# Kernel optimization log

Hardware: AMD Instinct MI355X
Metric: run time of the kernel (lower is better)

## Reference

```python
import jax, jax.numpy as jnp
import numpy as np

B, T, C, HS = 8, 4096, 1024, 64  # batch, seq, n_embd, head_size


def setup_inputs() -> dict:
    key = jax.random.key(0)
    kx, kk, kq, kv = jax.random.split(key, 4)
    x = jax.random.normal(kx, (B, T, C), dtype=jnp.float32)
    # bias-free linear weights, stored as [in, out] like flax kernels
    s = 1.0 / np.sqrt(C)
    Wk = jax.random.normal(kk, (C, HS), dtype=jnp.float32) * s
    Wq = jax.random.normal(kq, (C, HS), dtype=jnp.float32) * s
    Wv = jax.random.normal(kv, (C, HS), dtype=jnp.float32) * s
    return {"x": x, "Wk": Wk, "Wq": Wq, "Wv": Wv}


def reference(x, Wk, Wq, Wv):
    # x: [B, T, C]
    Tq = x.shape[1]
    Cdim = x.shape[2]
    k = jnp.einsum('btc,ch->bth', x, Wk)  # [B,T,HS]
    q = jnp.einsum('btc,ch->bth', x, Wq)
    v = jnp.einsum('btc,ch->bth', x, Wv)
    # NOTE: original scales by C**-0.5 (full embed dim), not head_size**-0.5
    scale = Cdim ** (-0.5)
    wei = jnp.einsum('bth,bsh->bts', q, k) * scale  # [B,T,T]
    causal = jnp.tril(jnp.ones((Tq, Tq), dtype=bool))
    wei = jnp.where(causal, wei, -jnp.inf)
    wei = jax.nn.softmax(wei, axis=-1)
    out = jnp.einsum('bts,bsh->bth', wei, v)  # [B,T,HS]
    return out
```

## Files before the change

kernel.cpp:

```cpp
#include <hip/hip_runtime.h>
#include <hip/hip_bf16.h>


typedef __attribute__((ext_vector_type(8))) short short8;
typedef __attribute__((ext_vector_type(4))) float f32x4;

#define NB 8
#define NT 4096
#define NC 1024
#define NH 64

__device__ __forceinline__ unsigned short f2bf(float f) {
    unsigned int u = __builtin_bit_cast(unsigned int, f);
    u += 0x7fffu + ((u >> 16) & 1u);
    return (unsigned short)(u >> 16);
}

__device__ __forceinline__ unsigned cvt_pk_bf16(float lo, float hi) {
    unsigned r;
    asm("v_cvt_pk_bf16_f32 %0, %1, %2" : "=v"(r) : "v"(lo), "v"(hi));
    return r;
}

#define GLOAD16(gp, lp)                                                        \
    __builtin_amdgcn_global_load_lds(                                          \
        (const __attribute__((address_space(1))) void*)(gp),                   \
        (__attribute__((address_space(3))) void*)(lp), 16, 0, 0)

__global__ __launch_bounds__(256) void wprep_kernel(
    const float* __restrict__ Wk, const float* __restrict__ Wq,
    const float* __restrict__ Wv, unsigned short* __restrict__ Wt)
{
    int n = blockIdx.x;
    int which = n >> 6, h = n & 63;
    const float* W = (which == 0) ? Wk : (which == 1) ? Wq : Wv;
    for (int c = threadIdx.x; c < NC; c += 256)
        Wt[(size_t)n * NC + c] = f2bf(W[(size_t)c * NH + h]);
}

__global__ __launch_bounds__(256, 2) void proj_kernel(
    const float* __restrict__ x, const unsigned short* __restrict__ Wt,
    unsigned short* __restrict__ qws, unsigned short* __restrict__ kws,
    unsigned short* __restrict__ vtws)
{
    __shared__ char lds[4][20480];

    const int lane = threadIdx.x & 63;
    const int wave = threadIdx.x >> 6;
    const int l15 = lane & 15;
    const int kg = lane >> 4;
    const int m0 = blockIdx.x * 64;

    const int agS = (lane & 7) ^ (lane >> 3);
    const float* aSrc[2];
#pragma unroll
    for (int j = 0; j < 2; ++j) {
        int i = wave * 2 + j;
        int r = 8 * i + (lane >> 3);
        aSrc[j] = x + (size_t)(m0 + r) * NC + agS * 4;
    }
    const int bgS = (lane & 3) ^ ((lane >> 2) & 3);
    const unsigned short* bSrc[3];
#pragma unroll
    for (int j = 0; j < 3; ++j) {
        int u = wave * 3 + j;
        int r = 16 * u + (lane >> 2);
        bSrc[j] = Wt + (size_t)r * NC + bgS * 8;
    }

    f32x4 acc[12];
#pragma unroll
    for (int i = 0; i < 12; ++i) acc[i] = f32x4{0.f, 0.f, 0.f, 0.f};

#define STAGE_CHUNK(c)                                                         \
    do {                                                                       \
        char* base_ = lds[(c) & 3];                                            \
        _Pragma("unroll")                                                      \
        for (int j = 0; j < 2; ++j)                                            \
            GLOAD16(aSrc[j] + (c) * 32, base_ + (wave * 2 + j) * 1024);        \
        _Pragma("unroll")                                                      \
        for (int j = 0; j < 3; ++j)                                            \
            GLOAD16(bSrc[j] + (c) * 32, base_ + 8192 + (wave * 3 + j) * 1024); \
    } while (0)

    STAGE_CHUNK(0);
    STAGE_CHUNK(1);

    for (int kc = 0; kc < 32; ++kc) {
        if (kc < 30) {
            STAGE_CHUNK(kc + 2);
            asm volatile("s_waitcnt vmcnt(10)" ::: "memory");
        } else if (kc == 30) {
            asm volatile("s_waitcnt vmcnt(5)" ::: "memory");
        } else {
            asm volatile("s_waitcnt vmcnt(0)" ::: "memory");
        }
        __builtin_amdgcn_sched_barrier(0);
        __builtin_amdgcn_s_barrier();

        const char* Ab = lds[kc & 3];
        const char* Bb = lds[kc & 3] + 8192;
        {
            const int r = wave * 16 + l15;
            const int g0 = kg * 2;
            f32x4 a0 = *(const f32x4*)(Ab + r * 128 + ((g0 ^ (r & 7)) * 16));
            f32x4 a1 = *(const f32x4*)(Ab + r * 128 + (((g0 + 1) ^ (r & 7)) * 16));
            short8 a;
            a[0] = (short)f2bf(a0[0]); a[1] = (short)f2bf(a0[1]);
            a[2] = (short)f2bf(a0[2]); a[3] = (short)f2bf(a0[3]);
            a[4] = (short)f2bf(a1[0]); a[5] = (short)f2bf(a1[1]);
            a[6] = (short)f2bf(a1[2]); a[7] = (short)f2bf(a1[3]);
#pragma unroll
            for (int nt = 0; nt < 12; ++nt) {
                int rb = nt * 16 + l15;
                short8 bfrag = *(const short8*)(
                    Bb + rb * 64 + ((kg ^ (rb & 3)) * 16));
                acc[nt] = __builtin_amdgcn_mfma_f32_16x16x32_bf16(a, bfrag, acc[nt], 0, 0, 0);
            }
        }
    }
#undef STAGE_CHUNK

    const float cs = 0.04508422f;
    const int crow0 = m0 + wave * 16 + (kg << 2);
#pragma unroll
    for (int nt = 0; nt < 12; ++nt) {
        int n = nt * 16 + l15;
        int which = n >> 6;
        int h = n & 63;
#pragma unroll
        for (int r = 0; r < 4; ++r) {
            int gm = crow0 + r;
            float av = acc[nt][r];
            if (which == 1) av *= cs;
            unsigned short v = f2bf(av);
            if (which == 0) {
                kws[(size_t)gm * NH + h] = v;
            } else if (which == 1) {
                qws[(size_t)gm * NH + h] = v;
            } else {
                int bb = gm >> 12, tt = gm & 4095;
                vtws[((size_t)(bb * NH + h)) * NT + tt] = v;
            }
        }
    }
}

__global__ __launch_bounds__(256) void flash_kernel(
    const unsigned short* __restrict__ qws, const unsigned short* __restrict__ kws,
    const unsigned short* __restrict__ vtws,
    float* __restrict__ opart, float* __restrict__ mlpart)
{
    __shared__ unsigned short Kbuf[2][64 * 64];
    __shared__ unsigned short Vbuf[2][64 * 64];
    __shared__ unsigned short Plds[4 * 16 * 64];

    const int id = blockIdx.x;
    const int kvh = id >> 9;
    const int rem9 = id & 511;
    const int lighthalf = rem9 >> 8;
    const int rem = rem9 & 255;
    const int b = rem & 7;
    const int i32 = rem >> 3;
    const int qt = lighthalf ? i32 : (63 - i32);
    const int nkv = qt + 1;
    const int hsp = nkv - (nkv >> 1);
    const int k0 = kvh ? hsp : 0;
    const int k1 = kvh ? nkv : hsp;
    const int pid_ = (kvh << 9) | ((b << 6) | qt);

    float* mlp = mlpart + (size_t)pid_ * 128;
    float* op  = opart + (size_t)pid_ * 4096;

    if (k0 >= k1) {
        f32x4 z = f32x4{0.f, 0.f, 0.f, 0.f};
        f32x4* op4 = (f32x4*)op;
        for (int i = threadIdx.x; i < 1024; i += 256) op4[i] = z;
        if (threadIdx.x < 64) {
            mlp[threadIdx.x] = -INFINITY;
            mlp[64 + threadIdx.x] = 0.f;
        }
        return;
    }

    const int lane = threadIdx.x & 63;
    const int wave = threadIdx.x >> 6;
    const int l15 = lane & 15;
    const int kg = lane >> 4;

    const int sg = (lane & 7) ^ (lane >> 3);
    const unsigned short* kSrc[2];
    const unsigned short* vSrc[2];
#pragma unroll
    for (int j = 0; j < 2; ++j) {
        int r = 16 * wave + 8 * j + (lane >> 3);
        kSrc[j] = kws + ((size_t)(b * NT) + r) * NH + sg * 8;
        vSrc[j] = vtws + ((size_t)(b * NH + r)) * NT + sg * 8;
    }

    short8 qf[2];
    {
        const unsigned short* qp =
            qws + ((size_t)(b * NT + qt * 64 + wave * 16 + l15)) * NH + kg * 8;
        qf[0] = *(const short8*)(qp);
        qf[1] = *(const short8*)(qp + 32);
    }

    f32x4 o[4];
#pragma unroll
    for (int dt = 0; dt < 4; ++dt) o[dt] = f32x4{0.f, 0.f, 0.f, 0.f};
    float m_r = -INFINITY;
    float l_r = 0.f;

    char* pw = (char*)Plds + wave * 2048;
    const int pswz = (l15 & 7) << 4;

#pragma unroll
    for (int j = 0; j < 2; ++j) {
        int i = 2 * wave + j;
        GLOAD16(kSrc[j] + (size_t)k0 * 64 * NH, (char*)Kbuf[0] + i * 1024);
        GLOAD16(vSrc[j] + (size_t)k0 * 64,      (char*)Vbuf[0] + i * 1024);
    }
    __syncthreads();

    int cur = 0;
    for (int kv = k0; kv < k1; ++kv) {
        if (kv + 1 < k1) {
#pragma unroll
            for (int j = 0; j < 2; ++j) {
                int i = 2 * wave + j;
                GLOAD16(kSrc[j] + (size_t)(kv + 1) * 64 * NH,
                        (char*)Kbuf[cur ^ 1] + i * 1024);
                GLOAD16(vSrc[j] + (size_t)(kv + 1) * 64,
                        (char*)Vbuf[cur ^ 1] + i * 1024);
            }
        }

        const char* Kb = (const char*)Kbuf[cur];
        const char* Vb = (const char*)Vbuf[cur];

        f32x4 st[4];
#pragma unroll
        for (int jt = 0; jt < 4; ++jt) st[jt] = f32x4{0.f, 0.f, 0.f, 0.f};
#pragma unroll
        for (int ks = 0; ks < 2; ++ks) {
            const int cbb = ks * 64 + kg * 16;
#pragma unroll
            for (int jt = 0; jt < 4; ++jt) {
                int krow = jt * 16 + l15;
                short8 kf = *(const short8*)(Kb + krow * 128 +
                                             (cbb ^ ((krow & 7) << 4)));
                st[jt] = __builtin_amdgcn_mfma_f32_16x16x32_bf16(kf, qf[ks], st[jt], 0, 0, 0);
            }
        }

        if (kv == qt) {
#pragma unroll
            for (int jt = 0; jt < 4; ++jt)
#pragma unroll
                for (int r = 0; r < 4; ++r)
                    if (jt * 16 + (kg << 2) + r > wave * 16 + l15)
                        st[jt][r] = -1e30f;
        }

        float lmax;
        {
            float t0 = fmaxf(fmaxf(st[0][0], st[0][1]), fmaxf(st[0][2], st[0][3]));
            float t1 = fmaxf(fmaxf(st[1][0], st[1][1]), fmaxf(st[1][2], st[1][3]));
            float t2 = fmaxf(fmaxf(st[2][0], st[2][1]), fmaxf(st[2][2], st[2][3]));
            float t3 = fmaxf(fmaxf(st[3][0], st[3][1]), fmaxf(st[3][2], st[3][3]));
            lmax = fmaxf(fmaxf(t0, t1), fmaxf(t2, t3));
        }

        if (!__all(lmax <= m_r + 8.0f)) {
            float pmax = lmax;
            pmax = fmaxf(pmax, __shfl_xor(pmax, 16));
            pmax = fmaxf(pmax, __shfl_xor(pmax, 32));
            float mn = fmaxf(m_r, pmax);
            float alpha = __builtin_amdgcn_exp2f(m_r - mn);
            m_r = mn;
            l_r *= alpha;
#pragma unroll
            for (int dt = 0; dt < 4; ++dt)
#pragma unroll
                for (int r = 0; r < 4; ++r)
                    o[dt][r] *= alpha;
        }

#pragma unroll
        for (int jt = 0; jt < 4; ++jt)
#pragma unroll
            for (int r = 0; r < 4; ++r)
                st[jt][r] = __builtin_amdgcn_exp2f(st[jt][r] - m_r);
        {
            float t0 = (st[0][0] + st[0][1]) + (st[0][2] + st[0][3]);
            float t1 = (st[1][0] + st[1][1]) + (st[1][2] + st[1][3]);
            float t2 = (st[2][0] + st[2][1]) + (st[2][2] + st[2][3]);
            float t3 = (st[3][0] + st[3][1]) + (st[3][2] + st[3][3]);
            l_r += (t0 + t1) + (t2 + t3);
        }

#pragma unroll
        for (int jt = 0; jt < 4; ++jt) {
            unsigned w0 = cvt_pk_bf16(st[jt][0], st[jt][1]);
            unsigned w1 = cvt_pk_bf16(st[jt][2], st[jt][3]);
            uint2 t; t.x = w0; t.y = w1;
            *(uint2*)(pw + l15 * 128 + ((jt * 32 + kg * 8) ^ pswz)) = t;
        }
        short8 pf[2];
#pragma unroll
        for (int ks = 0; ks < 2; ++ks)
            pf[ks] = *(const short8*)(pw + l15 * 128 + ((ks * 64 + kg * 16) ^ pswz));

#pragma unroll
        for (int ks = 0; ks < 2; ++ks) {
            const int cbb = ks * 64 + kg * 16;
#pragma unroll
            for (int dt = 0; dt < 4; ++dt) {
                int vrow = dt * 16 + l15;
                short8 vf = *(const short8*)(Vb + vrow * 128 +
                                             (cbb ^ ((vrow & 7) << 4)));
                o[dt] = __builtin_amdgcn_mfma_f32_16x16x32_bf16(vf, pf[ks], o[dt], 0, 0, 0);
            }
        }

        __syncthreads();
        cur ^= 1;
    }

    float lsum = l_r;
    lsum += __shfl_xor(lsum, 16);
    lsum += __shfl_xor(lsum, 32);
    float* orow = op + (wave * 16 + l15) * 64 + (kg << 2);
#pragma unroll
    for (int dt = 0; dt < 4; ++dt)
        *(f32x4*)(orow + dt * 16) = o[dt];
    if (kg == 0) {
        int q = wave * 16 + l15;
        mlp[q] = m_r;
        mlp[64 + q] = lsum;
    }
}

__global__ __launch_bounds__(256) void combine_kernel(
    const float* __restrict__ opart, const float* __restrict__ mlpart,
    float* __restrict__ out)
{
    const int cid = blockIdx.x;
    const int b = cid >> 6, qt = cid & 63;
    const float* mlA = mlpart + (size_t)cid * 128;
    const float* mlB = mlpart + (size_t)(512 + cid) * 128;
    const f32x4* oA = (const f32x4*)(opart + (size_t)cid * 4096);
    const f32x4* oB = (const f32x4*)(opart + (size_t)(512 + cid) * 4096);
    f32x4* og = (f32x4*)out;

#pragma unroll
    for (int i = 0; i < 4; ++i) {
        int g = threadIdx.x + i * 256;
        int row = g >> 4;
        float mA = mlA[row], lA = mlA[64 + row];
        float mB = mlB[row], lB = mlB[64 + row];
        float ms = fmaxf(mA, mB);
        float eA = __builtin_amdgcn_exp2f(mA - ms);
        float eB = __builtin_amdgcn_exp2f(mB - ms);
        float dinv = __builtin_amdgcn_rcpf(eA * lA + eB * lB);
        f32x4 a = oA[g], c = oB[g];
        f32x4 r;
        r[0] = (eA * a[0] + eB * c[0]) * dinv;
        r[1] = (eA * a[1] + eB * c[1]) * dinv;
        r[2] = (eA * a[2] + eB * c[2]) * dinv;
        r[3] = (eA * a[3] + eB * c[3]) * dinv;
        og[((size_t)(b * NT) + qt * 64 + row) * 16 + (g & 15)] = r;
    }
}

extern "C" void kernel_launch(void* const* d_in, const int* in_sizes, int n_in,
                              void* d_out, int out_size, void* d_ws, size_t ws_size,
                              hipStream_t stream) {
    const float* x  = (const float*)d_in[0];
    const float* Wk = (const float*)d_in[1];
    const float* Wq = (const float*)d_in[2];
    const float* Wv = (const float*)d_in[3];
    float* out = (float*)d_out;

    unsigned short* ws   = (unsigned short*)d_ws;
    const size_t qkv_elems = (size_t)NB * NT * NH;
    unsigned short* qws  = ws;
    unsigned short* kws  = qws + qkv_elems;
    unsigned short* vtws = kws + qkv_elems;
    unsigned short* Wt   = vtws + qkv_elems;
    float* opart  = (float*)(Wt + (size_t)192 * NC);
    float* mlpart = opart + (size_t)1024 * 4096;

    wprep_kernel<<<dim3(192), dim3(256), 0, stream>>>(Wk, Wq, Wv, Wt);
    proj_kernel<<<dim3(512), dim3(256), 0, stream>>>(x, Wt, qws, kws, vtws);
    flash_kernel<<<dim3(1024), dim3(256), 0, stream>>>(qws, kws, vtws, opart, mlpart);
    combine_kernel<<<dim3(512), dim3(256), 0, stream>>>(opart, mlpart, out);
}
```

Baseline: 86.96 us.

## Fuse split-KV combine into flash kernel via atomic last-arriver merge

New measurement: 242.1 us. 2.78x slower.

```diff
diff --git a/kernel.cpp b/kernel.cpp
--- a/kernel.cpp
+++ b/kernel.cpp
@@ -29,9 +29,11 @@
 
 __global__ __launch_bounds__(256) void wprep_kernel(
     const float* __restrict__ Wk, const float* __restrict__ Wq,
-    const float* __restrict__ Wv, unsigned short* __restrict__ Wt)
+    const float* __restrict__ Wv, unsigned short* __restrict__ Wt,
+    int* __restrict__ flags)
 {
     int n = blockIdx.x;
+    if (n < 2) flags[n * 256 + threadIdx.x] = 0;
     int which = n >> 6, h = n & 63;
     const float* W = (which == 0) ? Wk : (which == 1) ? Wq : Wv;
     for (int c = threadIdx.x; c < NC; c += 256)
@@ -149,11 +151,13 @@
 __global__ __launch_bounds__(256) void flash_kernel(
     const unsigned short* __restrict__ qws, const unsigned short* __restrict__ kws,
     const unsigned short* __restrict__ vtws,
-    float* __restrict__ opart, float* __restrict__ mlpart)
+    float* __restrict__ opart, float* __restrict__ mlpart,
+    int* __restrict__ flags, float* __restrict__ out)
 {
     __shared__ unsigned short Kbuf[2][64 * 64];
     __shared__ unsigned short Vbuf[2][64 * 64];
     __shared__ unsigned short Plds[4 * 16 * 64];
+    __shared__ int role;
 
     const int id = blockIdx.x;
     const int kvh = id >> 9;
@@ -172,17 +176,6 @@
     float* mlp = mlpart + (size_t)pid_ * 128;
     float* op  = opart + (size_t)pid_ * 4096;
 
-    if (k0 >= k1) {
-        f32x4 z = f32x4{0.f, 0.f, 0.f, 0.f};
-        f32x4* op4 = (f32x4*)op;
-        for (int i = threadIdx.x; i < 1024; i += 256) op4[i] = z;
-        if (threadIdx.x < 64) {
-            mlp[threadIdx.x] = -INFINITY;
-            mlp[64 + threadIdx.x] = 0.f;
-        }
-        return;
-    }
-
     const int lane = threadIdx.x & 63;
     const int wave = threadIdx.x >> 6;
     const int l15 = lane & 15;
@@ -215,11 +208,12 @@
     char* pw = (char*)Plds + wave * 2048;
     const int pswz = (l15 & 7) << 4;
 
+    const int kst = (k0 < 64) ? k0 : 63;
 #pragma unroll
     for (int j = 0; j < 2; ++j) {
         int i = 2 * wave + j;
-        GLOAD16(kSrc[j] + (size_t)k0 * 64 * NH, (char*)Kbuf[0] + i * 1024);
-        GLOAD16(vSrc[j] + (size_t)k0 * 64,      (char*)Vbuf[0] + i * 1024);
+        GLOAD16(kSrc[j] + (size_t)kst * 64 * NH, (char*)Kbuf[0] + i * 1024);
+        GLOAD16(vSrc[j] + (size_t)kst * 64,      (char*)Vbuf[0] + i * 1024);
     }
     __syncthreads();
 
@@ -242,6 +236,7 @@
         f32x4 st[4];
 #pragma unroll
         for (int jt = 0; jt < 4; ++jt) st[jt] = f32x4{0.f, 0.f, 0.f, 0.f};
+        __builtin_amdgcn_s_setprio(1);
 #pragma unroll
         for (int ks = 0; ks < 2; ++ks) {
             const int cbb = ks * 64 + kg * 16;
@@ -253,6 +248,7 @@
                 st[jt] = __builtin_amdgcn_mfma_f32_16x16x32_bf16(kf, qf[ks], st[jt], 0, 0, 0);
             }
         }
+        __builtin_amdgcn_s_setprio(0);
 
         if (kv == qt) {
 #pragma unroll
@@ -312,6 +308,7 @@
         for (int ks = 0; ks < 2; ++ks)
             pf[ks] = *(const short8*)(pw + l15 * 128 + ((ks * 64 + kg * 16) ^ pswz));
 
+        __builtin_amdgcn_s_setprio(1);
 #pragma unroll
         for (int ks = 0; ks < 2; ++ks) {
             const int cbb = ks * 64 + kg * 16;
@@ -323,6 +320,7 @@
                 o[dt] = __builtin_amdgcn_mfma_f32_16x16x32_bf16(vf, pf[ks], o[dt], 0, 0, 0);
             }
         }
+        __builtin_amdgcn_s_setprio(0);
 
         __syncthreads();
         cur ^= 1;
@@ -331,46 +329,43 @@
     float lsum = l_r;
     lsum += __shfl_xor(lsum, 16);
     lsum += __shfl_xor(lsum, 32);
-    float* orow = op + (wave * 16 + l15) * 64 + (kg << 2);
+    const int q = wave * 16 + l15;
+    float* orow = op + q * 64 + (kg << 2);
 #pragma unroll
     for (int dt = 0; dt < 4; ++dt)
         *(f32x4*)(orow + dt * 16) = o[dt];
     if (kg == 0) {
-        int q = wave * 16 + l15;
         mlp[q] = m_r;
         mlp[64 + q] = lsum;
     }
-}
-
-__global__ __launch_bounds__(256) void combine_kernel(
-    const float* __restrict__ opart, const float* __restrict__ mlpart,
-    float* __restrict__ out)
-{
-    const int cid = blockIdx.x;
-    const int b = cid >> 6, qt = cid & 63;
-    const float* mlA = mlpart + (size_t)cid * 128;
-    const float* mlB = mlpart + (size_t)(512 + cid) * 128;
-    const f32x4* oA = (const f32x4*)(opart + (size_t)cid * 4096);
-    const f32x4* oB = (const f32x4*)(opart + (size_t)(512 + cid) * 4096);
-    f32x4* og = (f32x4*)out;
-
-#pragma unroll
-    for (int i = 0; i < 4; ++i) {
-        int g = threadIdx.x + i * 256;
-        int row = g >> 4;
-        float mA = mlA[row], lA = mlA[64 + row];
-        float mB = mlB[row], lB = mlB[64 + row];
-        float ms = fmaxf(mA, mB);
-        float eA = __builtin_amdgcn_exp2f(mA - ms);
-        float eB = __builtin_amdgcn_exp2f(mB - ms);
-        float dinv = __builtin_amdgcn_rcpf(eA * lA + eB * lB);
-        f32x4 a = oA[g], c = oB[g];
-        f32x4 r;
-        r[0] = (eA * a[0] + eB * c[0]) * dinv;
-        r[1] = (eA * a[1] + eB * c[1]) * dinv;
-        r[2] = (eA * a[2] + eB * c[2]) * dinv;
-        r[3] = (eA * a[3] + eB * c[3]) * dinv;
-        og[((size_t)(b * NT) + qt * 64 + row) * 16 + (g & 15)] = r;
+
+    __threadfence();
+    __syncthreads();
+    if (threadIdx.x == 0)
+        role = atomicAdd(&flags[(b << 6) | qt], 1);
+    __syncthreads();
+    if (role == 0) return;
+
+    __threadfence();
+    const int partner = pid_ ^ (1 << 9);
+    const float* mlP = mlpart + (size_t)partner * 128;
+    const float* opP = opart + (size_t)partner * 4096;
+    float mP = mlP[q], lP = mlP[64 + q];
+    float ms = fmaxf(m_r, mP);
+    float eO = __builtin_amdgcn_exp2f(m_r - ms);
+    float eP = __builtin_amdgcn_exp2f(mP - ms);
+    float dinv = __builtin_amdgcn_rcpf(eO * lsum + eP * lP);
+    const float* prow = opP + q * 64 + (kg << 2);
+    float* grow = out + ((size_t)(b * NT) + qt * 64 + q) * NH + (kg << 2);
+#pragma unroll
+    for (int dt = 0; dt < 4; ++dt) {
+        f32x4 pv = *(const f32x4*)(prow + dt * 16);
+        f32x4 rr;
+        rr[0] = (eO * o[dt][0] + eP * pv[0]) * dinv;
+        rr[1] = (eO * o[dt][1] + eP * pv[1]) * dinv;
+        rr[2] = (eO * o[dt][2] + eP * pv[2]) * dinv;
+        rr[3] = (eO * o[dt][3] + eP * pv[3]) * dinv;
+        *(f32x4*)(grow + dt * 16) = rr;
     }
 }
 
@@ -391,9 +386,9 @@
     unsigned short* Wt   = vtws + qkv_elems;
     float* opart  = (float*)(Wt + (size_t)192 * NC);
     float* mlpart = opart + (size_t)1024 * 4096;
-
-    wprep_kernel<<<dim3(192), dim3(256), 0, stream>>>(Wk, Wq, Wv, Wt);
+    int*   flags  = (int*)(mlpart + (size_t)1024 * 128);
+
+    wprep_kernel<<<dim3(192), dim3(256), 0, stream>>>(Wk, Wq, Wv, Wt, flags);
     proj_kernel<<<dim3(512), dim3(256), 0, stream>>>(x, Wt, qws, kws, vtws);
-    flash_kernel<<<dim3(1024), dim3(256), 0, stream>>>(qws, kws, vtws, opart, mlpart);
-    combine_kernel<<<dim3(512), dim3(256), 0, stream>>>(opart, mlpart, out);
-}
+    flash_kernel<<<dim3(1024), dim3(256), 0, stream>>>(qws, kws, vtws, opart, mlpart, flags, out);
+}
```

## Use 32-wide KV tiles with 4-stage ring buffer and finer split-K balance

Applied to the files above, without the earlier changes.

Result: slower. 96.44 us (+10.9%).

```diff
diff --git a/kernel.cpp b/kernel.cpp
--- a/kernel.cpp
+++ b/kernel.cpp
@@ -151,9 +151,9 @@
     const unsigned short* __restrict__ vtws,
     float* __restrict__ opart, float* __restrict__ mlpart)
 {
-    __shared__ unsigned short Kbuf[2][64 * 64];
-    __shared__ unsigned short Vbuf[2][64 * 64];
-    __shared__ unsigned short Plds[4 * 16 * 64];
+    __shared__ unsigned short Kbuf[4][32 * 64];
+    __shared__ unsigned short Vbuf[4][64 * 32];
+    __shared__ unsigned short Plds[4][16 * 32];
 
     const int id = blockIdx.x;
     const int kvh = id >> 9;
@@ -163,40 +163,24 @@
     const int b = rem & 7;
     const int i32 = rem >> 3;
     const int qt = lighthalf ? i32 : (63 - i32);
-    const int nkv = qt + 1;
-    const int hsp = nkv - (nkv >> 1);
-    const int k0 = kvh ? hsp : 0;
-    const int k1 = kvh ? nkv : hsp;
+    const int k0 = kvh ? (qt + 1) : 0;
+    const int k1 = kvh ? (2 * qt + 2) : (qt + 1);
     const int pid_ = (kvh << 9) | ((b << 6) | qt);
 
     float* mlp = mlpart + (size_t)pid_ * 128;
     float* op  = opart + (size_t)pid_ * 4096;
-
-    if (k0 >= k1) {
-        f32x4 z = f32x4{0.f, 0.f, 0.f, 0.f};
-        f32x4* op4 = (f32x4*)op;
-        for (int i = threadIdx.x; i < 1024; i += 256) op4[i] = z;
-        if (threadIdx.x < 64) {
-            mlp[threadIdx.x] = -INFINITY;
-            mlp[64 + threadIdx.x] = 0.f;
-        }
-        return;
-    }
 
     const int lane = threadIdx.x & 63;
     const int wave = threadIdx.x >> 6;
     const int l15 = lane & 15;
     const int kg = lane >> 4;
 
-    const int sg = (lane & 7) ^ (lane >> 3);
-    const unsigned short* kSrc[2];
-    const unsigned short* vSrc[2];
-#pragma unroll
-    for (int j = 0; j < 2; ++j) {
-        int r = 16 * wave + 8 * j + (lane >> 3);
-        kSrc[j] = kws + ((size_t)(b * NT) + r) * NH + sg * 8;
-        vSrc[j] = vtws + ((size_t)(b * NH + r)) * NT + sg * 8;
-    }
+    const unsigned short* kSrc =
+        kws + ((size_t)(b * NT) + 8 * wave + (lane >> 3)) * NH +
+        (((lane & 7) ^ (lane >> 3)) * 8);
+    const unsigned short* vSrc =
+        vtws + ((size_t)(b * NH) + 16 * wave + (lane >> 2)) * NT +
+        (((lane & 3) ^ ((lane >> 2) & 3)) * 8);
 
     short8 qf[2];
     {
@@ -205,6 +189,7 @@
         qf[0] = *(const short8*)(qp);
         qf[1] = *(const short8*)(qp + 32);
     }
+    asm volatile("s_waitcnt vmcnt(0)" ::: "memory");
 
     f32x4 o[4];
 #pragma unroll
@@ -212,54 +197,56 @@
     float m_r = -INFINITY;
     float l_r = 0.f;
 
-    char* pw = (char*)Plds + wave * 2048;
-    const int pswz = (l15 & 7) << 4;
-
-#pragma unroll
-    for (int j = 0; j < 2; ++j) {
-        int i = 2 * wave + j;
-        GLOAD16(kSrc[j] + (size_t)k0 * 64 * NH, (char*)Kbuf[0] + i * 1024);
-        GLOAD16(vSrc[j] + (size_t)k0 * 64,      (char*)Vbuf[0] + i * 1024);
-    }
-    __syncthreads();
-
-    int cur = 0;
+    char* pw = (char*)Plds[wave];
+    const int qbw = qt * 64 + wave * 16;
+
+#define STAGE_KV(t)                                                            \
+    do {                                                                       \
+        GLOAD16(kSrc + (size_t)(t) * 32 * NH, (char*)Kbuf[(t) & 3] + wave * 1024); \
+        GLOAD16(vSrc + (t) * 32,              (char*)Vbuf[(t) & 3] + wave * 1024); \
+    } while (0)
+
+    STAGE_KV(k0);
+    if (k0 + 1 < k1) STAGE_KV(k0 + 1);
+
     for (int kv = k0; kv < k1; ++kv) {
-        if (kv + 1 < k1) {
-#pragma unroll
-            for (int j = 0; j < 2; ++j) {
-                int i = 2 * wave + j;
-                GLOAD16(kSrc[j] + (size_t)(kv + 1) * 64 * NH,
-                        (char*)Kbuf[cur ^ 1] + i * 1024);
-                GLOAD16(vSrc[j] + (size_t)(kv + 1) * 64,
-                        (char*)Vbuf[cur ^ 1] + i * 1024);
-            }
-        }
-
-        const char* Kb = (const char*)Kbuf[cur];
-        const char* Vb = (const char*)Vbuf[cur];
-
-        f32x4 st[4];
-#pragma unroll
-        for (int jt = 0; jt < 4; ++jt) st[jt] = f32x4{0.f, 0.f, 0.f, 0.f};
+        if (kv + 2 < k1) {
+            STAGE_KV(kv + 2);
+            asm volatile("s_waitcnt vmcnt(4)" ::: "memory");
+        } else if (kv + 1 < k1) {
+            asm volatile("s_waitcnt vmcnt(2)" ::: "memory");
+        } else {
+            asm volatile("s_waitcnt vmcnt(0)" ::: "memory");
+        }
+        __builtin_amdgcn_sched_barrier(0);
+        __builtin_amdgcn_s_barrier();
+
+        const char* Kb = (const char*)Kbuf[kv & 3];
+        const char* Vb = (const char*)Vbuf[kv & 3];
+
+        f32x4 st[2];
+        st[0] = f32x4{0.f, 0.f, 0.f, 0.f};
+        st[1] = f32x4{0.f, 0.f, 0.f, 0.f};
+        __builtin_amdgcn_s_setprio(1);
 #pragma unroll
         for (int ks = 0; ks < 2; ++ks) {
-            const int cbb = ks * 64 + kg * 16;
-#pragma unroll
-            for (int jt = 0; jt < 4; ++jt) {
+            const int cg = ks * 4 + kg;
+#pragma unroll
+            for (int jt = 0; jt < 2; ++jt) {
                 int krow = jt * 16 + l15;
                 short8 kf = *(const short8*)(Kb + krow * 128 +
-                                             (cbb ^ ((krow & 7) << 4)));
+                                             ((cg ^ (krow & 7)) << 4));
                 st[jt] = __builtin_amdgcn_mfma_f32_16x16x32_bf16(kf, qf[ks], st[jt], 0, 0, 0);
             }
         }
-
-        if (kv == qt) {
-#pragma unroll
-            for (int jt = 0; jt < 4; ++jt)
+        __builtin_amdgcn_s_setprio(0);
+
+        if (kv * 32 + 31 > qbw) {
+#pragma unroll
+            for (int jt = 0; jt < 2; ++jt)
 #pragma unroll
                 for (int r = 0; r < 4; ++r)
-                    if (jt * 16 + (kg << 2) + r > wave * 16 + l15)
+                    if (kv * 32 + jt * 16 + (kg << 2) + r > qbw + l15)
                         st[jt][r] = -1e30f;
         }
 
@@ -267,9 +254,7 @@
         {
             float t0 = fmaxf(fmaxf(st[0][0], st[0][1]), fmaxf(st[0][2], st[0][3]));
             float t1 = fmaxf(fmaxf(st[1][0], st[1][1]), fmaxf(st[1][2], st[1][3]));
-            float t2 = fmaxf(fmaxf(st[2][0], st[2][1]), fmaxf(st[2][2], st[2][3]));
-            float t3 = fmaxf(fmaxf(st[3][0], st[3][1]), fmaxf(st[3][2], st[3][3]));
-            lmax = fmaxf(fmaxf(t0, t1), fmaxf(t2, t3));
+            lmax = fmaxf(t0, t1);
         }
 
         if (!__all(lmax <= m_r + 8.0f)) {
@@ -288,55 +273,44 @@
         }
 
 #pragma unroll
-        for (int jt = 0; jt < 4; ++jt)
+        for (int jt = 0; jt < 2; ++jt)
 #pragma unroll
             for (int r = 0; r < 4; ++r)
                 st[jt][r] = __builtin_amdgcn_exp2f(st[jt][r] - m_r);
-        {
-            float t0 = (st[0][0] + st[0][1]) + (st[0][2] + st[0][3]);
-            float t1 = (st[1][0] + st[1][1]) + (st[1][2] + st[1][3]);
-            float t2 = (st[2][0] + st[2][1]) + (st[2][2] + st[2][3]);
-            float t3 = (st[3][0] + st[3][1]) + (st[3][2] + st[3][3]);
-            l_r += (t0 + t1) + (t2 + t3);
-        }
-
-#pragma unroll
-        for (int jt = 0; jt < 4; ++jt) {
-            unsigned w0 = cvt_pk_bf16(st[jt][0], st[jt][1]);
-            unsigned w1 = cvt_pk_bf16(st[jt][2], st[jt][3]);
-            uint2 t; t.x = w0; t.y = w1;
-            *(uint2*)(pw + l15 * 128 + ((jt * 32 + kg * 8) ^ pswz)) = t;
-        }
-        short8 pf[2];
-#pragma unroll
-        for (int ks = 0; ks < 2; ++ks)
-            pf[ks] = *(const short8*)(pw + l15 * 128 + ((ks * 64 + kg * 16) ^ pswz));
-
-#pragma unroll
-        for (int ks = 0; ks < 2; ++ks) {
-            const int cbb = ks * 64 + kg * 16;
-#pragma unroll
-            for (int dt = 0; dt < 4; ++dt) {
-                int vrow = dt * 16 + l15;
-                short8 vf = *(const short8*)(Vb + vrow * 128 +
-                                             (cbb ^ ((vrow & 7) << 4)));
-                o[dt] = __builtin_amdgcn_mfma_f32_16x16x32_bf16(vf, pf[ks], o[dt], 0, 0, 0);
-            }
-        }
-
-        __syncthreads();
-        cur ^= 1;
-    }
+        l_r += ((st[0][0] + st[0][1]) + (st[0][2] + st[0][3])) +
+               ((st[1][0] + st[1][1]) + (st[1][2] + st[1][3]));
+
+#pragma unroll
+        for (int jt = 0; jt < 2; ++jt) {
+            uint2 t;
+            t.x = cvt_pk_bf16(st[jt][0], st[jt][1]);
+            t.y = cvt_pk_bf16(st[jt][2], st[jt][3]);
+            int phys = (jt * 2 + (kg >> 1)) ^ (l15 & 3);
+            *(uint2*)(pw + l15 * 64 + (phys << 4) + ((kg & 1) << 3)) = t;
+        }
+        short8 pf = *(const short8*)(pw + l15 * 64 + (((kg ^ (l15 & 3))) << 4));
+
+        __builtin_amdgcn_s_setprio(1);
+#pragma unroll
+        for (int dt = 0; dt < 4; ++dt) {
+            int vrow = dt * 16 + l15;
+            short8 vf = *(const short8*)(Vb + vrow * 64 +
+                                         (((kg ^ (vrow & 3))) << 4));
+            o[dt] = __builtin_amdgcn_mfma_f32_16x16x32_bf16(vf, pf, o[dt], 0, 0, 0);
+        }
+        __builtin_amdgcn_s_setprio(0);
+    }
+#undef STAGE_KV
 
     float lsum = l_r;
     lsum += __shfl_xor(lsum, 16);
     lsum += __shfl_xor(lsum, 32);
-    float* orow = op + (wave * 16 + l15) * 64 + (kg << 2);
+    const int q = wave * 16 + l15;
+    float* orow = op + q * 64 + (kg << 2);
 #pragma unroll
     for (int dt = 0; dt < 4; ++dt)
         *(f32x4*)(orow + dt * 16) = o[dt];
     if (kg == 0) {
-        int q = wave * 16 + l15;
         mlp[q] = m_r;
         mlp[64 + q] = lsum;
     }
```

## Split only heavy query tiles across KV halves; write light tiles directly

Applied to the files above, without the earlier changes.

Result: no change. 86.44 us (-0.6%).

```diff
diff --git a/kernel.cpp b/kernel.cpp
--- a/kernel.cpp
+++ b/kernel.cpp
@@ -149,38 +149,34 @@
 __global__ __launch_bounds__(256) void flash_kernel(
     const unsigned short* __restrict__ qws, const unsigned short* __restrict__ kws,
     const unsigned short* __restrict__ vtws,
-    float* __restrict__ opart, float* __restrict__ mlpart)
+    float* __restrict__ opart, float* __restrict__ mlpart,
+    float* __restrict__ out)
 {
     __shared__ unsigned short Kbuf[2][64 * 64];
     __shared__ unsigned short Vbuf[2][64 * 64];
     __shared__ unsigned short Plds[4 * 16 * 64];
 
     const int id = blockIdx.x;
-    const int kvh = id >> 9;
-    const int rem9 = id & 511;
-    const int lighthalf = rem9 >> 8;
-    const int rem = rem9 & 255;
-    const int b = rem & 7;
-    const int i32 = rem >> 3;
-    const int qt = lighthalf ? i32 : (63 - i32);
-    const int nkv = qt + 1;
-    const int hsp = nkv - (nkv >> 1);
-    const int k0 = kvh ? hsp : 0;
-    const int k1 = kvh ? nkv : hsp;
-    const int pid_ = (kvh << 9) | ((b << 6) | qt);
-
-    float* mlp = mlpart + (size_t)pid_ * 128;
-    float* op  = opart + (size_t)pid_ * 4096;
-
-    if (k0 >= k1) {
-        f32x4 z = f32x4{0.f, 0.f, 0.f, 0.f};
-        f32x4* op4 = (f32x4*)op;
-        for (int i = threadIdx.x; i < 1024; i += 256) op4[i] = z;
-        if (threadIdx.x < 64) {
-            mlp[threadIdx.x] = -INFINITY;
-            mlp[64 + threadIdx.x] = 0.f;
-        }
-        return;
+    int b, qt, k0, k1, pid;
+    bool direct;
+    if (id < 512) {
+        direct = false;
+        const int j = id >> 4;
+        qt = 63 - j;
+        const int half = (id >> 3) & 1;
+        b = id & 7;
+        const int nkv = qt + 1;
+        const int hsp = nkv - (nkv >> 1);
+        k0 = half ? hsp : 0;
+        k1 = half ? nkv : hsp;
+        pid = ((31 - j) << 4) | (half << 3) | b;
+    } else {
+        direct = true;
+        const int r = id - 512;
+        qt = 31 - (r >> 3);
+        b = r & 7;
+        k0 = 0; k1 = qt + 1;
+        pid = 0;
     }
 
     const int lane = threadIdx.x & 63;
@@ -242,6 +238,7 @@
         f32x4 st[4];
 #pragma unroll
         for (int jt = 0; jt < 4; ++jt) st[jt] = f32x4{0.f, 0.f, 0.f, 0.f};
+        __builtin_amdgcn_s_setprio(1);
 #pragma unroll
         for (int ks = 0; ks < 2; ++ks) {
             const int cbb = ks * 64 + kg * 16;
@@ -253,6 +250,7 @@
                 st[jt] = __builtin_amdgcn_mfma_f32_16x16x32_bf16(kf, qf[ks], st[jt], 0, 0, 0);
             }
         }
+        __builtin_amdgcn_s_setprio(0);
 
         if (kv == qt) {
 #pragma unroll
@@ -312,6 +310,7 @@
         for (int ks = 0; ks < 2; ++ks)
             pf[ks] = *(const short8*)(pw + l15 * 128 + ((ks * 64 + kg * 16) ^ pswz));
 
+        __builtin_amdgcn_s_setprio(1);
 #pragma unroll
         for (int ks = 0; ks < 2; ++ks) {
             const int cbb = ks * 64 + kg * 16;
@@ -323,6 +322,7 @@
                 o[dt] = __builtin_amdgcn_mfma_f32_16x16x32_bf16(vf, pf[ks], o[dt], 0, 0, 0);
             }
         }
+        __builtin_amdgcn_s_setprio(0);
 
         __syncthreads();
         cur ^= 1;
@@ -331,14 +331,28 @@
     float lsum = l_r;
     lsum += __shfl_xor(lsum, 16);
     lsum += __shfl_xor(lsum, 32);
-    float* orow = op + (wave * 16 + l15) * 64 + (kg << 2);
-#pragma unroll
-    for (int dt = 0; dt < 4; ++dt)
-        *(f32x4*)(orow + dt * 16) = o[dt];
-    if (kg == 0) {
-        int q = wave * 16 + l15;
-        mlp[q] = m_r;
-        mlp[64 + q] = lsum;
+    const int q = wave * 16 + l15;
+
+    if (direct) {
+        float linv = __builtin_amdgcn_rcpf(lsum);
+        float* grow = out + ((size_t)(b * NT) + qt * 64 + q) * NH + (kg << 2);
+#pragma unroll
+        for (int dt = 0; dt < 4; ++dt) {
+            f32x4 v = o[dt];
+            v[0] *= linv; v[1] *= linv; v[2] *= linv; v[3] *= linv;
+            *(f32x4*)(grow + dt * 16) = v;
+        }
+    } else {
+        float* op = opart + (size_t)pid * 4096;
+        float* mlp = mlpart + (size_t)pid * 128;
+        float* orow = op + q * 64 + (kg << 2);
+#pragma unroll
+        for (int dt = 0; dt < 4; ++dt)
+            *(f32x4*)(orow + dt * 16) = o[dt];
+        if (kg == 0) {
+            mlp[q] = m_r;
+            mlp[64 + q] = lsum;
+        }
     }
 }
 
@@ -347,11 +361,14 @@
     float* __restrict__ out)
 {
     const int cid = blockIdx.x;
-    const int b = cid >> 6, qt = cid & 63;
-    const float* mlA = mlpart + (size_t)cid * 128;
-    const float* mlB = mlpart + (size_t)(512 + cid) * 128;
-    const f32x4* oA = (const f32x4*)(opart + (size_t)cid * 4096);
-    const f32x4* oB = (const f32x4*)(opart + (size_t)(512 + cid) * 4096);
+    const int qti = cid >> 3, b = cid & 7;
+    const int qt = qti + 32;
+    const int pidA = (qti << 4) | b;
+    const int pidB = (qti << 4) | 8 | b;
+    const float* mlA = mlpart + (size_t)pidA * 128;
+    const float* mlB = mlpart + (size_t)pidB * 128;
+    const f32x4* oA = (const f32x4*)(opart + (size_t)pidA * 4096);
+    const f32x4* oB = (const f32x4*)(opart + (size_t)pidB * 4096);
     f32x4* og = (f32x4*)out;
 
 #pragma unroll
@@ -390,10 +407,10 @@
     unsigned short* vtws = kws + qkv_elems;
     unsigned short* Wt   = vtws + qkv_elems;
     float* opart  = (float*)(Wt + (size_t)192 * NC);
-    float* mlpart = opart + (size_t)1024 * 4096;
+    float* mlpart = opart + (size_t)512 * 4096;
 
     wprep_kernel<<<dim3(192), dim3(256), 0, stream>>>(Wk, Wq, Wv, Wt);
     proj_kernel<<<dim3(512), dim3(256), 0, stream>>>(x, Wt, qws, kws, vtws);
-    flash_kernel<<<dim3(1024), dim3(256), 0, stream>>>(qws, kws, vtws, opart, mlpart);
-    combine_kernel<<<dim3(512), dim3(256), 0, stream>>>(opart, mlpart, out);
-}
+    flash_kernel<<<dim3(768), dim3(256), 0, stream>>>(qws, kws, vtws, opart, mlpart, out);
+    combine_kernel<<<dim3(256), dim3(256), 0, stream>>>(opart, mlpart, out);
+}
```
